# Performance work log

Measured on AMD Instinct MI355X. Metric: run time of the kernel, lower is better.

## Reference

```python
import jax, jax.numpy as jnp
import numpy as np

TEMPERATURE = 0.5
NEG_INF = -1e30


def setup_inputs() -> dict:
    key = jax.random.key(0)
    batch_size, k, d = 2048, 4, 256
    features = jax.random.normal(key, (batch_size * k, d), dtype=jnp.float32)
    return {"features": features, "batch_size": batch_size, "k": k}


def reference(features, batch_size, k):
    n = batch_size * k
    f = features.reshape(n, -1)
    f = f / jnp.linalg.norm(f, axis=1, keepdims=True)
    sim = jnp.matmul(f, f.T) / TEMPERATURE  # [N, N]

    gid = jnp.arange(n) // k
    eye = jnp.eye(n, dtype=bool)
    pos_mask = (gid[:, None] == gid[None, :]) & ~eye  # same image, not self
    all_mask = ~eye  # positives + negatives (everything except self)

    lse_pos = jax.nn.logsumexp(jnp.where(pos_mask, sim, NEG_INF), axis=1)
    lse_all = jax.nn.logsumexp(jnp.where(all_mask, sim, NEG_INF), axis=1)
    # every row has k-1 >= 1 positives, so all queries contribute
    return jnp.mean(-(lse_pos - lse_all))
```

## Files before the change

### kernel.cpp

```cpp
#include <hip/hip_runtime.h>
#include <math.h>

#define NROW 8192
#define DIM 256
#define NTILE 64
#define NBLK 2080
#define NT 24

typedef float f32x4  __attribute__((ext_vector_type(4)));
typedef short short8 __attribute__((ext_vector_type(8)));

__device__ __forceinline__ ushort f2bf_rne(float x) {
    unsigned u = __float_as_uint(x);
    unsigned r = (u + 0x7FFFu + ((u >> 16) & 1u)) >> 16;
    return (ushort)r;
}
__device__ __forceinline__ float bf2f(ushort h) {
    return __uint_as_float(((unsigned)h) << 16);
}

__global__ __launch_bounds__(256) void prep_kernel(const float* __restrict__ f,
                                                   ushort* __restrict__ Hi,
                                                   ushort* __restrict__ Lo,
                                                   float* __restrict__ sums) {
    if (threadIdx.x < 8) sums[blockIdx.x * 8 + threadIdx.x] = 0.0f;
    const int row = blockIdx.x * 4 + (threadIdx.x >> 6);
    const int l   = threadIdx.x & 63;
    float4 v = reinterpret_cast<const float4*>(f + (size_t)row * DIM)[l];
    float ss = v.x * v.x + v.y * v.y + v.z * v.z + v.w * v.w;
#pragma unroll
    for (int m = 32; m; m >>= 1) ss += __shfl_xor(ss, m, 64);
    const float inv = 1.0f / sqrtf(ss);
    float xv[4] = {v.x * inv, v.y * inv, v.z * inv, v.w * inv};
    ushort hv[4], lv[4];
#pragma unroll
    for (int i = 0; i < 4; ++i) {
        hv[i] = f2bf_rne(xv[i]);
        lv[i] = f2bf_rne(xv[i] - bf2f(hv[i]));
    }
    size_t idx = (size_t)((row >> 4) * 32 + (l >> 1)) * 128 + (row & 15) * 8 + (l & 1) * 4;
    *reinterpret_cast<ushort4*>(&Hi[idx]) = make_ushort4(hv[0], hv[1], hv[2], hv[3]);
    *reinterpret_cast<ushort4*>(&Lo[idx]) = make_ushort4(lv[0], lv[1], lv[2], lv[3]);
}

__device__ __forceinline__ void gload16(const void* g, void* lp) {
    __builtin_amdgcn_global_load_lds((__attribute__((address_space(1))) void*)g,
                                     (__attribute__((address_space(3))) void*)lp, 16, 0, 0);
}

__global__ __launch_bounds__(256, 3) void infonce_mfma(const ushort* __restrict__ Hi,
                                                       const ushort* __restrict__ Lo,
                                                       float* __restrict__ all_sum,
                                                       float* __restrict__ pos_sum) {
    __shared__ ushort lds[3][2][4096];

    int ti = 0, rem = blockIdx.x;
    while (rem >= NTILE - ti) { rem -= NTILE - ti; ++ti; }
    const int tj = ti + rem;

    const int tid = threadIdx.x;
    const int wid = tid >> 6, l = tid & 63;
    const int wr = wid >> 1, wc = wid & 1;

    f32x4 acc[4][4];
#pragma unroll
    for (int m = 0; m < 4; ++m)
#pragma unroll
        for (int n = 0; n < 4; ++n) acc[m][n] = (f32x4){0.f, 0.f, 0.f, 0.f};

#define STAGE(bufi, t) do {                                                             \
        const int pass_ = (t) >> 3, kk_ = (t) & 7;                                      \
        const ushort* As_ = (pass_ == 2) ? Lo : Hi;                                     \
        const ushort* Bs_ = (pass_ == 1) ? Lo : Hi;                                     \
        const int f0_ = wid * 2, f1_ = f0_ + 1;                                         \
        gload16(&As_[(size_t)((ti * 8 + f0_) * 4096 + kk_ * 512) + l * 8],              \
                &lds[bufi][0][f0_ * 512 + l * 8]);                                      \
        gload16(&As_[(size_t)((ti * 8 + f1_) * 4096 + kk_ * 512) + l * 8],              \
                &lds[bufi][0][f1_ * 512 + l * 8]);                                      \
        gload16(&Bs_[(size_t)((tj * 8 + f0_) * 4096 + kk_ * 512) + l * 8],              \
                &lds[bufi][1][f0_ * 512 + l * 8]);                                      \
        gload16(&Bs_[(size_t)((tj * 8 + f1_) * 4096 + kk_ * 512) + l * 8],              \
                &lds[bufi][1][f1_ * 512 + l * 8]);                                      \
    } while (0)

#define VWAIT(n) asm volatile("s_waitcnt vmcnt(" #n ")" ::: "memory")

#define BODY(t, bR, bS) do {                                                            \
        short8 af_[4], bf_[4];                                                          \
        _Pragma("unroll") for (int m = 0; m < 4; ++m)                                   \
            af_[m] = *reinterpret_cast<const short8*>(&lds[bR][0][(wr * 4 + m) * 512 + l * 8]); \
        _Pragma("unroll") for (int n = 0; n < 4; ++n)                                   \
            bf_[n] = *reinterpret_cast<const short8*>(&lds[bR][1][(wc * 4 + n) * 512 + l * 8]); \
        if ((t) + 2 < NT) STAGE(bS, (t) + 2);                                           \
        __builtin_amdgcn_s_setprio(1);                                                  \
        _Pragma("unroll") for (int m = 0; m < 4; ++m)                                   \
            _Pragma("unroll") for (int n = 0; n < 4; ++n)                               \
                acc[m][n] = __builtin_amdgcn_mfma_f32_16x16x32_bf16(af_[m], bf_[n], acc[m][n], 0, 0, 0); \
        __builtin_amdgcn_s_setprio(0);                                                  \
        if ((t) + 2 < NT) { VWAIT(4); } else { VWAIT(0); }                              \
        __builtin_amdgcn_s_barrier();                                                   \
    } while (0)

    STAGE(0, 0);
    STAGE(1, 1);
    VWAIT(4);
    __builtin_amdgcn_s_barrier();

#pragma unroll 1
    for (int tb = 0; tb < NT; tb += 3) {
        BODY(tb + 0, 0, 2);
        BODY(tb + 1, 1, 0);
        BODY(tb + 2, 2, 1);
    }

    const int rbase = ti * 128 + wr * 64;
    const int cbase = tj * 128 + wc * 64;
    const int h = l >> 4, c16 = l & 15;

    if (ti == tj) {
#pragma unroll
        for (int m = 0; m < 4; ++m)
#pragma unroll
            for (int e = 0; e < 4; ++e) {
                const int row = rbase + m * 16 + h * 4 + e;
                float asum = 0.f, psum = 0.f;
#pragma unroll
                for (int n = 0; n < 4; ++n) {
                    const int col = cbase + n * 16 + c16;
                    float v = __expf(2.0f * acc[m][n][e]);
                    v = (row == col) ? 0.f : v;
                    asum += v;
                    psum += ((row >> 2) == (col >> 2)) ? v : 0.f;
                }
#pragma unroll
                for (int mk = 1; mk < 16; mk <<= 1) {
                    asum += __shfl_xor(asum, mk, 64);
                    psum += __shfl_xor(psum, mk, 64);
                }
                if (c16 == 0) {
                    atomicAdd(&all_sum[row], asum);
                    atomicAdd(&pos_sum[row], psum);
                }
            }
    } else {
        float csum[4] = {0.f, 0.f, 0.f, 0.f};
#pragma unroll
        for (int m = 0; m < 4; ++m)
#pragma unroll
            for (int e = 0; e < 4; ++e) {
                const int row = rbase + m * 16 + h * 4 + e;
                float asum = 0.f;
#pragma unroll
                for (int n = 0; n < 4; ++n) {
                    float v = __expf(2.0f * acc[m][n][e]);
                    asum += v;
                    csum[n] += v;
                }
#pragma unroll
                for (int mk = 1; mk < 16; mk <<= 1) asum += __shfl_xor(asum, mk, 64);
                if (c16 == 0) atomicAdd(&all_sum[row], asum);
            }
#pragma unroll
        for (int n = 0; n < 4; ++n) {
            float cs = csum[n];
            cs += __shfl_xor(cs, 16, 64);
            cs += __shfl_xor(cs, 32, 64);
            if (h == 0) atomicAdd(&all_sum[cbase + n * 16 + c16], cs);
        }
    }
#undef STAGE
#undef VWAIT
#undef BODY
}

__global__ __launch_bounds__(1024) void loss_kernel(const float* __restrict__ all_sum,
                                                    const float* __restrict__ pos_sum,
                                                    float* __restrict__ out) {
    const int tid = threadIdx.x;
    float s = 0.0f;
#pragma unroll
    for (int r = 0; r < 8; ++r) {
        const int i = tid + r * 1024;
        s += __logf(all_sum[i]) - __logf(pos_sum[i]);
    }
#pragma unroll
    for (int off = 32; off; off >>= 1) s += __shfl_xor(s, off, 64);
    __shared__ float red[16];
    if ((tid & 63) == 0) red[tid >> 6] = s;
    __syncthreads();
    if (tid == 0) {
        float tot = 0.f;
#pragma unroll
        for (int i = 0; i < 16; ++i) tot += red[i];
        out[0] = tot / (float)NROW;
    }
}

extern "C" void kernel_launch(void* const* d_in, const int* in_sizes, int n_in,
                              void* d_out, int out_size, void* d_ws, size_t ws_size,
                              hipStream_t stream) {
    const float* f = (const float*)d_in[0];
    float* out = (float*)d_out;

    float*  all_sum = (float*)d_ws;
    float*  pos_sum = all_sum + NROW;
    ushort* Hi      = (ushort*)(pos_sum + NROW);
    ushort* Lo      = Hi + (size_t)NROW * DIM;

    prep_kernel<<<NROW / 4, 256, 0, stream>>>(f, Hi, Lo, all_sum);
    infonce_mfma<<<NBLK, 256, 0, stream>>>(Hi, Lo, all_sum, pos_sum);
    loss_kernel<<<1, 1024, 0, stream>>>(all_sum, pos_sum, out);
}
```

Measured before the change: 141.6 us.

## Fuse loss reduction into GEMM kernel, stage prep output in LDS, swizzle tiles

The final loss reduction moves into the main MFMA kernel as a last-block-done pattern using an atomic counter, which removes one kernel launch. The prep kernel now handles 32 rows per block, builds the tiled bf16 hi/lo layout in shared memory and writes it out with coalesced stores. Blocks are remapped through an XCD-style swizzle before triangular tile decoding, and the k-loop tail is peeled so the wait counts are constant at compile time. In exchange, every block pays a threadfence and an atomic, and the last block serially reduces 8192 logs.

```diff
diff --git a/kernel.cpp b/kernel.cpp
--- a/kernel.cpp
+++ b/kernel.cpp
@@ -22,25 +22,42 @@
 __global__ __launch_bounds__(256) void prep_kernel(const float* __restrict__ f,
                                                    ushort* __restrict__ Hi,
                                                    ushort* __restrict__ Lo,
-                                                   float* __restrict__ sums) {
-    if (threadIdx.x < 8) sums[blockIdx.x * 8 + threadIdx.x] = 0.0f;
-    const int row = blockIdx.x * 4 + (threadIdx.x >> 6);
-    const int l   = threadIdx.x & 63;
-    float4 v = reinterpret_cast<const float4*>(f + (size_t)row * DIM)[l];
-    float ss = v.x * v.x + v.y * v.y + v.z * v.z + v.w * v.w;
-#pragma unroll
-    for (int m = 32; m; m >>= 1) ss += __shfl_xor(ss, m, 64);
-    const float inv = 1.0f / sqrtf(ss);
-    float xv[4] = {v.x * inv, v.y * inv, v.z * inv, v.w * inv};
-    ushort hv[4], lv[4];
-#pragma unroll
-    for (int i = 0; i < 4; ++i) {
-        hv[i] = f2bf_rne(xv[i]);
-        lv[i] = f2bf_rne(xv[i] - bf2f(hv[i]));
-    }
-    size_t idx = (size_t)((row >> 4) * 32 + (l >> 1)) * 128 + (row & 15) * 8 + (l & 1) * 4;
-    *reinterpret_cast<ushort4*>(&Hi[idx]) = make_ushort4(hv[0], hv[1], hv[2], hv[3]);
-    *reinterpret_cast<ushort4*>(&Lo[idx]) = make_ushort4(lv[0], lv[1], lv[2], lv[3]);
+                                                   float* __restrict__ sums,
+                                                   unsigned* __restrict__ done) {
+    __shared__ ushort hbuf[8192];
+    __shared__ ushort lbuf[8192];
+    const int tid = threadIdx.x;
+    if (tid < 64) sums[blockIdx.x * 64 + tid] = 0.0f;
+    if (blockIdx.x == 0 && tid == 0) *done = 0u;
+    const int w = tid >> 6, l = tid & 63;
+    const int r0 = blockIdx.x * 32;
+#pragma unroll
+    for (int it = 0; it < 8; ++it) {
+        const int rl = it * 4 + w;
+        float4 v = reinterpret_cast<const float4*>(f + (size_t)(r0 + rl) * DIM)[l];
+        float ss = v.x * v.x + v.y * v.y + v.z * v.z + v.w * v.w;
+#pragma unroll
+        for (int m = 32; m; m >>= 1) ss += __shfl_xor(ss, m, 64);
+        const float inv = 1.0f / sqrtf(ss);
+        float xv[4] = {v.x * inv, v.y * inv, v.z * inv, v.w * inv};
+        ushort hv[4], lv[4];
+#pragma unroll
+        for (int i = 0; i < 4; ++i) {
+            hv[i] = f2bf_rne(xv[i]);
+            lv[i] = f2bf_rne(xv[i] - bf2f(hv[i]));
+        }
+        const int pos = (rl >> 4) * 4096 + (l >> 1) * 128 + (rl & 15) * 8 + (l & 1) * 4;
+        *reinterpret_cast<ushort4*>(&hbuf[pos]) = make_ushort4(hv[0], hv[1], hv[2], hv[3]);
+        *reinterpret_cast<ushort4*>(&lbuf[pos]) = make_ushort4(lv[0], lv[1], lv[2], lv[3]);
+    }
+    __syncthreads();
+    const size_t gbase = (size_t)blockIdx.x * 8192;
+#pragma unroll
+    for (int it = 0; it < 8; ++it) {
+        const int o = it * 1024 + tid * 4;
+        *reinterpret_cast<ushort4*>(&Hi[gbase + o]) = *reinterpret_cast<const ushort4*>(&hbuf[o]);
+        *reinterpret_cast<ushort4*>(&Lo[gbase + o]) = *reinterpret_cast<const ushort4*>(&lbuf[o]);
+    }
 }
 
 __device__ __forceinline__ void gload16(const void* g, void* lp) {
@@ -51,10 +68,15 @@
 __global__ __launch_bounds__(256, 3) void infonce_mfma(const ushort* __restrict__ Hi,
                                                        const ushort* __restrict__ Lo,
                                                        float* __restrict__ all_sum,
-                                                       float* __restrict__ pos_sum) {
+                                                       float* __restrict__ pos_sum,
+                                                       unsigned* __restrict__ done,
+                                                       float* __restrict__ out) {
     __shared__ ushort lds[3][2][4096];
-
-    int ti = 0, rem = blockIdx.x;
+    __shared__ float red[4];
+    __shared__ bool lastBlock;
+
+    const int swz = (blockIdx.x & 7) * 260 + (blockIdx.x >> 3);
+    int ti = 0, rem = swz;
     while (rem >= NTILE - ti) { rem -= NTILE - ti; ++ti; }
     const int tj = ti + rem;
 
@@ -85,19 +107,19 @@
 
 #define VWAIT(n) asm volatile("s_waitcnt vmcnt(" #n ")" ::: "memory")
 
-#define BODY(t, bR, bS) do {                                                            \
+#define BODY(t, bR, bS, DOSTG, W) do {                                                  \
         short8 af_[4], bf_[4];                                                          \
         _Pragma("unroll") for (int m = 0; m < 4; ++m)                                   \
             af_[m] = *reinterpret_cast<const short8*>(&lds[bR][0][(wr * 4 + m) * 512 + l * 8]); \
         _Pragma("unroll") for (int n = 0; n < 4; ++n)                                   \
             bf_[n] = *reinterpret_cast<const short8*>(&lds[bR][1][(wc * 4 + n) * 512 + l * 8]); \
-        if ((t) + 2 < NT) STAGE(bS, (t) + 2);                                           \
+        if (DOSTG) STAGE(bS, (t) + 2);                                                  \
         __builtin_amdgcn_s_setprio(1);                                                  \
         _Pragma("unroll") for (int m = 0; m < 4; ++m)                                   \
             _Pragma("unroll") for (int n = 0; n < 4; ++n)                               \
                 acc[m][n] = __builtin_amdgcn_mfma_f32_16x16x32_bf16(af_[m], bf_[n], acc[m][n], 0, 0, 0); \
         __builtin_amdgcn_s_setprio(0);                                                  \
-        if ((t) + 2 < NT) { VWAIT(4); } else { VWAIT(0); }                              \
+        VWAIT(W);                                                                       \
         __builtin_amdgcn_s_barrier();                                                   \
     } while (0)
 
@@ -107,11 +129,14 @@
     __builtin_amdgcn_s_barrier();
 
 #pragma unroll 1
-    for (int tb = 0; tb < NT; tb += 3) {
-        BODY(tb + 0, 0, 2);
-        BODY(tb + 1, 1, 0);
-        BODY(tb + 2, 2, 1);
-    }
+    for (int tb = 0; tb < 21; tb += 3) {
+        BODY(tb + 0, 0, 2, 1, 4);
+        BODY(tb + 1, 1, 0, 1, 4);
+        BODY(tb + 2, 2, 1, 1, 4);
+    }
+    BODY(21, 0, 2, 1, 4);
+    BODY(22, 1, 0, 0, 0);
+    BODY(23, 2, 0, 0, 0);
 
     const int rbase = ti * 128 + wr * 64;
     const int cbase = tj * 128 + wc * 64;
@@ -168,32 +193,28 @@
             if (h == 0) atomicAdd(&all_sum[cbase + n * 16 + c16], cs);
         }
     }
+
+    __threadfence();
+    if (tid == 0) {
+        unsigned old = atomicAdd(done, 1u);
+        lastBlock = (old == NBLK - 1);
+    }
+    __syncthreads();
+    if (lastBlock) {
+        __threadfence();
+        float s = 0.0f;
+#pragma unroll 4
+        for (int i = tid; i < NROW; i += 256)
+            s += __logf(all_sum[i]) - __logf(pos_sum[i]);
+#pragma unroll
+        for (int off = 32; off; off >>= 1) s += __shfl_xor(s, off, 64);
+        if (l == 0) red[wid] = s;
+        __syncthreads();
+        if (tid == 0) out[0] = (red[0] + red[1] + red[2] + red[3]) / (float)NROW;
+    }
 #undef STAGE
 #undef VWAIT
 #undef BODY
-}
-
-__global__ __launch_bounds__(1024) void loss_kernel(const float* __restrict__ all_sum,
-                                                    const float* __restrict__ pos_sum,
-                                                    float* __restrict__ out) {
-    const int tid = threadIdx.x;
-    float s = 0.0f;
-#pragma unroll
-    for (int r = 0; r < 8; ++r) {
-        const int i = tid + r * 1024;
-        s += __logf(all_sum[i]) - __logf(pos_sum[i]);
-    }
-#pragma unroll
-    for (int off = 32; off; off >>= 1) s += __shfl_xor(s, off, 64);
-    __shared__ float red[16];
-    if ((tid & 63) == 0) red[tid >> 6] = s;
-    __syncthreads();
-    if (tid == 0) {
-        float tot = 0.f;
-#pragma unroll
-        for (int i = 0; i < 16; ++i) tot += red[i];
-        out[0] = tot / (float)NROW;
-    }
 }
 
 extern "C" void kernel_launch(void* const* d_in, const int* in_sizes, int n_in,
@@ -202,12 +223,12 @@
     const float* f = (const float*)d_in[0];
     float* out = (float*)d_out;
 
-    float*  all_sum = (float*)d_ws;
-    float*  pos_sum = all_sum + NROW;
-    ushort* Hi      = (ushort*)(pos_sum + NROW);
-    ushort* Lo      = Hi + (size_t)NROW * DIM;
-
-    prep_kernel<<<NROW / 4, 256, 0, stream>>>(f, Hi, Lo, all_sum);
-    infonce_mfma<<<NBLK, 256, 0, stream>>>(Hi, Lo, all_sum, pos_sum);
-    loss_kernel<<<1, 1024, 0, stream>>>(all_sum, pos_sum, out);
-}
+    float*    all_sum = (float*)d_ws;
+    float*    pos_sum = all_sum + NROW;
+    unsigned* done    = (unsigned*)(pos_sum + NROW);
+    ushort*   Hi      = (ushort*)(pos_sum + NROW + 4);
+    ushort*   Lo      = Hi + (size_t)NROW * DIM;
+
+    prep_kernel<<<NROW / 32, 256, 0, stream>>>(f, Hi, Lo, all_sum, done);
+    infonce_mfma<<<NBLK, 256, 0, stream>>>(Hi, Lo, all_sum, pos_sum, done, out);
+}
```

Result: slower. 275.3 us (+94.3%).
